# Optimization experiments

Measured on AMD Instinct MI355X. Metric: run time of the kernel, lower is better.

The kernel has to match this reference:

```python
import jax, jax.numpy as jnp
import numpy as np

B, V = 256, 128000


def setup_inputs() -> dict:
    key = jax.random.key(0)
    k1, k2, k3, k4, k5 = jax.random.split(key, 5)
    logits = jax.random.normal(k1, (B, V), dtype=jnp.float32) * 2.0
    temperatures = jax.random.uniform(k2, (B,), dtype=jnp.float32, minval=0.5, maxval=1.5)
    top_ps = jax.random.uniform(k3, (B,), dtype=jnp.float32, minval=0.7, maxval=1.0)
    top_ks = jax.random.randint(k4, (B,), 1, 101, dtype=jnp.int32)
    min_ps = jax.random.uniform(k5, (B,), dtype=jnp.float32, minval=0.0, maxval=0.1)
    return {"logits": logits, "temperatures": temperatures, "top_ps": top_ps,
            "top_ks": top_ks, "min_ps": min_ps}


def reference(logits, temperatures, top_ps, top_ks, min_ps):
    # temperature scaling + softmax (forward path with is_all_greedy=False)
    logits = logits.astype(jnp.float32) / temperatures[:, None]
    probs = jax.nn.softmax(logits, axis=-1)  # [B, V]

    # descending sort of probabilities, keep permutation for un-sorting
    order = jnp.argsort(-probs, axis=-1)                      # [B, V]
    probs_sort = jnp.take_along_axis(probs, order, axis=-1)   # [B, V]
    csum = jnp.cumsum(probs_sort, axis=-1)                    # cumsum BEFORE masking (matches torch)

    ranks = jnp.arange(V, dtype=jnp.int32)[None, :]
    probs_sort = jnp.where(ranks >= top_ks[:, None], 0.0, probs_sort)          # top-k mask
    probs_sort = jnp.where(csum - probs_sort > top_ps[:, None], 0.0, probs_sort)  # top-p mask
    # need_min_p_sampling=False in forward, so min_ps is unused (kept for signature parity)

    # multinomial(num_samples=1) over unnormalized masked probs == categorical on log-weights
    logw = jnp.where(probs_sort > 0, jnp.log(probs_sort), -jnp.inf)
    sampled = jax.random.categorical(jax.random.key(42), logw, axis=-1)  # [B]
    next_ids = jnp.take_along_axis(order, sampled[:, None], axis=-1).reshape(-1)
    return next_ids
```

## Files before the change

### kernel.cpp

```cpp
#include <hip/hip_runtime.h>
#include <stdint.h>
#include <math.h>

#define BB 256
#define VV 128000
#define NV4 (VV / 4)
#define NHALF4 (NV4 / 2)
#define CAPG 512
#define KMAX 100
#define TPB 1024
#define TPC 512
#define THR 6.0f
#define LOG2E 1.4426950408889634f

#define WS_CNT_OFF 0
#define WS_Z_OFF 1024
#define WS_CL_OFF 3072
#define WS_CI_OFF (3072 + BB * CAPG * 4)
#define WS_NEED (size_t)(3072 + BB * CAPG * 8)

__device__ __forceinline__ uint32_t threefry_xor_bits(uint32_t x0, uint32_t x1) {
    const uint32_t k0 = 0u, k1 = 42u;
    const uint32_t k2 = k0 ^ k1 ^ 0x1BD11BDAu;
    uint32_t ks[3] = {k0, k1, k2};
    const int rotA[4] = {13, 15, 26, 6};
    const int rotB[4] = {17, 29, 16, 24};
    x0 += ks[0];
    x1 += ks[1];
#pragma unroll
    for (int g = 0; g < 5; g++) {
        const int* rot = (g & 1) ? rotB : rotA;
#pragma unroll
        for (int i = 0; i < 4; i++) {
            x0 += x1;
            x1 = (x1 << rot[i]) | (x1 >> (32 - rot[i]));
            x1 ^= x0;
        }
        x0 += ks[(g + 1) % 3];
        x1 += ks[(g + 2) % 3] + (uint32_t)(g + 1);
    }
    return x0 ^ x1;
}

__device__ __forceinline__ float wave_maxf(float v) {
    for (int s = 32; s > 0; s >>= 1) v = fmaxf(v, __shfl_down(v, s));
    return v;
}
__device__ __forceinline__ float wave_sumf(float v) {
    for (int s = 32; s > 0; s >>= 1) v += __shfl_down(v, s);
    return v;
}

__device__ void common_tail(int b, int tid, const float* sort_p, const int* sort_idx,
                            float* csum_s, float* red_val, int* red_idx,
                            float topp, int topk, int* out) {
    if (tid == 0) {
        float c = 0.f;
        for (int r = 0; r < KMAX; r++) {
            c += sort_p[r];
            csum_s[r] = c;
        }
    }
    __syncthreads();
    float val = -INFINITY;
    if (tid < KMAX && tid < topk) {
        float p = sort_p[tid];
        if (!(csum_s[tid] - p > topp)) {
            float lw = logf(p);
            uint32_t idx = (uint32_t)b * (uint32_t)VV + (uint32_t)tid;
            uint32_t bits = threefry_xor_bits(0u, idx);
            uint32_t fb = (bits >> 9) | 0x3F800000u;
            float f = __uint_as_float(fb) - 1.0f;
            const float TINY = 1.17549435082228751e-38f;
            float u = fmaxf(TINY, __fadd_rn(__fmul_rn(f, 1.0f - TINY), TINY));
            float g = -logf(-logf(u));
            val = g + lw;
        }
    }
    if (tid < 128) {
        red_val[tid] = (tid < KMAX) ? val : -INFINITY;
        red_idx[tid] = tid;
    }
    __syncthreads();
    for (int s = 64; s > 0; s >>= 1) {
        if (tid < s) {
            float v1 = red_val[tid], v2 = red_val[tid + s];
            int i1 = red_idx[tid], i2 = red_idx[tid + s];
            if (v2 > v1 || (v2 == v1 && i2 < i1)) {
                red_val[tid] = v2;
                red_idx[tid] = i2;
            }
        }
        __syncthreads();
    }
    if (tid == 0) out[b] = sort_idx[red_idx[0]];
}

template <int NT>
__device__ void fallback_fill(const float* row, float T, int tid,
                              float* wv, int* iwv, float* sort_p, int* sort_idx,
                              float* s_f , int* s_i ) {
    const int lane = tid & 63, wave = tid >> 6;
    const int NW = NT / 64;
    float lm = -INFINITY;
    for (int j = tid; j < VV; j += NT) lm = fmaxf(lm, row[j]);
    lm = wave_maxf(lm);
    if (lane == 0) wv[wave] = lm;
    __syncthreads();
    if (tid == 0) {
        float M = wv[0];
        for (int w = 1; w < NW; w++) M = fmaxf(M, wv[w]);
        s_f[0] = M;
    }
    __syncthreads();
    const float m = s_f[0] / T;
    float zp = 0.f;
    for (int j = tid; j < VV; j += NT) zp += expf(row[j] / T - m);
    zp = wave_sumf(zp);
    __syncthreads();
    if (lane == 0) wv[wave] = zp;
    __syncthreads();
    if (tid == 0) {
        float Zs = wv[0];
        for (int w = 1; w < NW; w++) Zs += wv[w];
        s_f[1] = Zs;
    }
    __syncthreads();
    const float Z = s_f[1];
    float prevP = INFINITY;
    int prevJ = -1;
    for (int r = 0; r < KMAX; r++) {
        float bp = -1.f;
        int bj = 0x7FFFFFFF;
        for (int j = tid; j < VV; j += NT) {
            float p = expf(row[j] / T - m);
            bool elig = (p < prevP) || (p == prevP && j > prevJ);
            if (elig && (p > bp || (p == bp && j < bj))) {
                bp = p;
                bj = j;
            }
        }
        for (int s = 32; s > 0; s >>= 1) {
            float op = __shfl_down(bp, s);
            int oj = __shfl_down(bj, s);
            if (op > bp || (op == bp && oj < bj)) {
                bp = op;
                bj = oj;
            }
        }
        if (lane == 0) {
            wv[wave] = bp;
            iwv[wave] = bj;
        }
        __syncthreads();
        if (tid == 0) {
            float P = wv[0];
            int J = iwv[0];
            for (int w = 1; w < NW; w++)
                if (wv[w] > P || (wv[w] == P && iwv[w] < J)) {
                    P = wv[w];
                    J = iwv[w];
                }
            sort_p[r] = P / Z;
            sort_idx[r] = J;
            s_f[1] = P;
            s_i[0] = J;
        }
        __syncthreads();
        prevP = s_f[1];
        prevJ = s_i[0];
        __syncthreads();
    }
}

__global__ void init_kernel(int* wcnt) {
    if (threadIdx.x < BB) wcnt[threadIdx.x] = 0;
}

__global__ __launch_bounds__(TPB, 8) void pass_kernel(
    const float* __restrict__ logits, const float* __restrict__ temps,
    int* __restrict__ wcnt, float* __restrict__ wz,
    float* __restrict__ wcl, int* __restrict__ wci) {
    __shared__ float wv[TPB / 64];
    const int blk = blockIdx.x;
    const int b = blk >> 1, half = blk & 1;
    const int tid = threadIdx.x, lane = tid & 63, wave = tid >> 6;
    const float T = temps[b];
    const float c1 = LOG2E / T;
    const float4* row4 = (const float4*)(logits + (size_t)b * VV) + half * NHALF4;
    const int base4 = half * NHALF4;

    float z = 0.f;
    int i = tid;
    for (; i + 3 * TPB < NHALF4; i += 4 * TPB) {
        float4 v0 = row4[i];
        float4 v1 = row4[i + TPB];
        float4 v2 = row4[i + 2 * TPB];
        float4 v3 = row4[i + 3 * TPB];
        float a[16] = {v0.x, v0.y, v0.z, v0.w, v1.x, v1.y, v1.z, v1.w,
                       v2.x, v2.y, v2.z, v2.w, v3.x, v3.y, v3.z, v3.w};
#pragma unroll
        for (int j = 0; j < 16; j++) {
            float l = a[j];
            z += exp2f(l * c1);
            if (l >= THR) {
                int slot = atomicAdd(&wcnt[b], 1);
                if (slot < CAPG) {
                    wcl[b * CAPG + slot] = l;
                    wci[b * CAPG + slot] = (base4 + i + (j >> 2) * TPB) * 4 + (j & 3);
                }
            }
        }
    }
    for (; i < NHALF4; i += TPB) {
        float4 v = row4[i];
        float a[4] = {v.x, v.y, v.z, v.w};
#pragma unroll
        for (int j = 0; j < 4; j++) {
            float l = a[j];
            z += exp2f(l * c1);
            if (l >= THR) {
                int slot = atomicAdd(&wcnt[b], 1);
                if (slot < CAPG) {
                    wcl[b * CAPG + slot] = l;
                    wci[b * CAPG + slot] = (base4 + i) * 4 + j;
                }
            }
        }
    }
    z = wave_sumf(z);
    if (lane == 0) wv[wave] = z;
    __syncthreads();
    if (tid == 0) {
        float Z = wv[0];
        for (int w = 1; w < TPB / 64; w++) Z += wv[w];
        wz[2 * b + half] = Z;
    }
}

__global__ __launch_bounds__(TPC) void tail_kernel(
    const float* __restrict__ logits, const float* __restrict__ temps,
    const float* __restrict__ top_ps, const int* __restrict__ top_ks,
    const int* __restrict__ wcnt, const float* __restrict__ wz,
    const float* __restrict__ wcl, const int* __restrict__ wci,
    int* __restrict__ out) {
    __shared__ float cand_p[CAPG];
    __shared__ int cand_i[CAPG];
    __shared__ float sort_p[KMAX];
    __shared__ int sort_idx[KMAX];
    __shared__ float csum_s[KMAX];
    __shared__ float red_val[128];
    __shared__ int red_idx[128];
    __shared__ float wv[TPC / 64];
    __shared__ int iwv[TPC / 64];
    __shared__ float s_f[2];
    __shared__ int s_i[1];

    const int b = blockIdx.x, tid = threadIdx.x, lane = tid & 63, wave = tid >> 6;
    const float T = temps[b];
    const float c1 = LOG2E / T;
    const int cnt = wcnt[b];
    const float* row = logits + (size_t)b * VV;

    if (cnt >= KMAX && cnt <= CAPG) {
        const int C = cnt;
        float myl = -INFINITY;
        int myi = 0;
        if (tid < C) {
            myl = wcl[b * CAPG + tid];
            myi = wci[b * CAPG + tid];
        }
        float v = wave_maxf(myl);
        if (lane == 0) wv[wave] = v;
        __syncthreads();
        if (tid == 0) {
            float M = wv[0];
            for (int w = 1; w < TPC / 64; w++) M = fmaxf(M, wv[w]);
            s_f[0] = M;
        }
        __syncthreads();
        const float lmax = s_f[0];
        const float m = lmax / T;
        const float Z = (wz[2 * b] + wz[2 * b + 1]) * exp2f(-lmax * c1);
        float my_pn = 0.f;
        if (tid < C) {
            float x = myl / T;
            float p = expf(x - m);
            my_pn = p / Z;
            cand_p[tid] = my_pn;
            cand_i[tid] = myi;
        }
        __syncthreads();
        if (tid < C) {
            int r = 0;
            for (int c = 0; c < C; c++) {
                float pc = cand_p[c];
                int ic = cand_i[c];
                if (pc > my_pn || (pc == my_pn && ic < myi)) r++;
            }
            if (r < KMAX) {
                sort_p[r] = my_pn;
                sort_idx[r] = myi;
            }
        }
        __syncthreads();
    } else {
        fallback_fill<TPC>(row, T, tid, wv, iwv, sort_p, sort_idx, s_f, s_i);
    }

    common_tail(b, tid, sort_p, sort_idx, csum_s, red_val, red_idx,
                top_ps[b], top_ks[b], out);
}

__global__ __launch_bounds__(TPB) void fused_kernel(
    const float* __restrict__ logits, const float* __restrict__ temps,
    const float* __restrict__ top_ps, const int* __restrict__ top_ks,
    int* __restrict__ out) {
    __shared__ float cl[CAPG];
    __shared__ int ci[CAPG];
    __shared__ float cand_p[CAPG];
    __shared__ int cand_i[CAPG];
    __shared__ float sort_p[KMAX];
    __shared__ int sort_idx[KMAX];
    __shared__ float csum_s[KMAX];
    __shared__ float red_val[128];
    __shared__ int red_idx[128];
    __shared__ float wv[TPB / 64];
    __shared__ int iwv[TPB / 64];
    __shared__ float s_f[2];
    __shared__ int s_i[1];
    __shared__ int s_cnt;

    const int b = blockIdx.x, tid = threadIdx.x, lane = tid & 63, wave = tid >> 6;
    const float T = temps[b];
    const float c1 = LOG2E / T;
    const float* row = logits + (size_t)b * VV;
    const float4* row4 = (const float4*)row;

    if (tid == 0) s_cnt = 0;
    __syncthreads();
    float z = 0.f, lmax = -INFINITY;
    for (int i = tid; i < NV4; i += TPB) {
        float4 v = row4[i];
        float a[4] = {v.x, v.y, v.z, v.w};
#pragma unroll
        for (int j = 0; j < 4; j++) {
            float l = a[j];
            lmax = fmaxf(lmax, l);
            z += exp2f(l * c1);
            if (l >= THR) {
                int slot = atomicAdd(&s_cnt, 1);
                if (slot < CAPG) {
                    cl[slot] = l;
                    ci[slot] = i * 4 + j;
                }
            }
        }
    }
    lmax = wave_maxf(lmax);
    if (lane == 0) wv[wave] = lmax;
    __syncthreads();
    if (tid == 0) {
        float M = wv[0];
        for (int w = 1; w < TPB / 64; w++) M = fmaxf(M, wv[w]);
        s_f[0] = M;
    }
    __syncthreads();
    const float lm = s_f[0];
    z = wave_sumf(z);
    __syncthreads();
    if (lane == 0) wv[wave] = z;
    __syncthreads();
    if (tid == 0) {
        float Zs = wv[0];
        for (int w = 1; w < TPB / 64; w++) Zs += wv[w];
        s_f[1] = Zs;
    }
    __syncthreads();
    const float Zraw = s_f[1];
    const int cnt = s_cnt;
    __syncthreads();

    if (cnt >= KMAX && cnt <= CAPG) {
        const int C = cnt;
        const float m = lm / T;
        const float Z = Zraw * exp2f(-lm * c1);
        float my_pn = 0.f;
        int myi = 0;
        if (tid < C) {
            float x = cl[tid] / T;
            float p = expf(x - m);
            my_pn = p / Z;
            myi = ci[tid];
            cand_p[tid] = my_pn;
            cand_i[tid] = myi;
        }
        __syncthreads();
        if (tid < C) {
            int r = 0;
            for (int c = 0; c < C; c++) {
                float pc = cand_p[c];
                int icx = cand_i[c];
                if (pc > my_pn || (pc == my_pn && icx < myi)) r++;
            }
            if (r < KMAX) {
                sort_p[r] = my_pn;
                sort_idx[r] = myi;
            }
        }
        __syncthreads();
    } else {
        fallback_fill<TPB>(row, T, tid, wv, iwv, sort_p, sort_idx, s_f, s_i);
    }

    common_tail(b, tid, sort_p, sort_idx, csum_s, red_val, red_idx,
                top_ps[b], top_ks[b], out);
}

extern "C" void kernel_launch(void* const* d_in, const int* in_sizes, int n_in,
                              void* d_out, int out_size, void* d_ws, size_t ws_size,
                              hipStream_t stream) {
    const float* logits = (const float*)d_in[0];
    const float* temps = (const float*)d_in[1];
    const float* top_ps = (const float*)d_in[2];
    const int* top_ks = (const int*)d_in[3];
    int* out = (int*)d_out;

    if (ws_size >= WS_NEED) {
        char* wsb = (char*)d_ws;
        int* wcnt = (int*)(wsb + WS_CNT_OFF);
        float* wz = (float*)(wsb + WS_Z_OFF);
        float* wcl = (float*)(wsb + WS_CL_OFF);
        int* wci = (int*)(wsb + WS_CI_OFF);
        init_kernel<<<1, 256, 0, stream>>>(wcnt);
        pass_kernel<<<BB * 2, TPB, 0, stream>>>(logits, temps, wcnt, wz, wcl, wci);
        tail_kernel<<<BB, TPC, 0, stream>>>(logits, temps, top_ps, top_ks,
                                            wcnt, wz, wcl, wci, out);
    } else {
        fused_kernel<<<BB, TPB, 0, stream>>>(logits, temps, top_ps, top_ks, out);
    }
}
```

Before: 238.8 us.

## Split rows into eight slices with shared-memory candidate buffers, drop init kernel

The pass kernel now splits each row into eight slices handled by 256-thread blocks instead of two halves on 1024-thread blocks. Candidates above the threshold are gathered into per-block shared memory with shared atomics, then written out with per-slice counts. This removes global atomics and the separate init kernel. A max-of-16 early check skips the per-element candidate test for most groups. The tail kernel merges the eight slice lists and sums eight partial Z values, which adds a little serial work per row.

```diff
diff --git a/kernel.cpp b/kernel.cpp
--- a/kernel.cpp
+++ b/kernel.cpp
@@ -5,19 +5,23 @@
 #define BB 256
 #define VV 128000
 #define NV4 (VV / 4)
-#define NHALF4 (NV4 / 2)
+#define SLICES 8
+#define SLICE_E (VV / SLICES)
+#define SLICE_F4 (SLICE_E / 4)
+#define SL 320
 #define CAPG 512
 #define KMAX 100
+#define TPP 256
+#define TPC 512
 #define TPB 1024
-#define TPC 512
 #define THR 6.0f
 #define LOG2E 1.4426950408889634f
 
 #define WS_CNT_OFF 0
-#define WS_Z_OFF 1024
-#define WS_CL_OFF 3072
-#define WS_CI_OFF (3072 + BB * CAPG * 4)
-#define WS_NEED (size_t)(3072 + BB * CAPG * 8)
+#define WS_Z_OFF 8192
+#define WS_CL_OFF 16384
+#define WS_CI_OFF (16384 + 2048 * SL * 4)
+#define WS_NEED (size_t)(16384 + (size_t)2048 * SL * 8)
 
 __device__ __forceinline__ uint32_t threefry_xor_bits(uint32_t x0, uint32_t x1) {
     const uint32_t k0 = 0u, k1 = 42u;
@@ -99,7 +103,7 @@
 template <int NT>
 __device__ void fallback_fill(const float* row, float T, int tid,
                               float* wv, int* iwv, float* sort_p, int* sort_idx,
-                              float* s_f , int* s_i ) {
+                              float* s_f, int* s_i) {
     const int lane = tid & 63, wave = tid >> 6;
     const int NW = NT / 64;
     float lm = -INFINITY;
@@ -173,68 +177,89 @@
     }
 }
 
-__global__ void init_kernel(int* wcnt) {
-    if (threadIdx.x < BB) wcnt[threadIdx.x] = 0;
-}
-
-__global__ __launch_bounds__(TPB, 8) void pass_kernel(
+__global__ __launch_bounds__(TPP, 8) void pass_kernel(
     const float* __restrict__ logits, const float* __restrict__ temps,
     int* __restrict__ wcnt, float* __restrict__ wz,
     float* __restrict__ wcl, int* __restrict__ wci) {
-    __shared__ float wv[TPB / 64];
+    __shared__ float scl[SL];
+    __shared__ int sci[SL];
+    __shared__ float wvv[TPP / 64];
+    __shared__ int s_cnt;
+
     const int blk = blockIdx.x;
-    const int b = blk >> 1, half = blk & 1;
+    const int b = blk >> 3, sl = blk & 7;
     const int tid = threadIdx.x, lane = tid & 63, wave = tid >> 6;
     const float T = temps[b];
     const float c1 = LOG2E / T;
-    const float4* row4 = (const float4*)(logits + (size_t)b * VV) + half * NHALF4;
-    const int base4 = half * NHALF4;
+    const float4* row4 = (const float4*)(logits + (size_t)b * VV) + sl * SLICE_F4;
+    const int ebase = sl * SLICE_E;
+
+    if (tid == 0) s_cnt = 0;
+    __syncthreads();
 
     float z = 0.f;
     int i = tid;
-    for (; i + 3 * TPB < NHALF4; i += 4 * TPB) {
+    for (; i + 3 * TPP < SLICE_F4; i += 4 * TPP) {
         float4 v0 = row4[i];
-        float4 v1 = row4[i + TPB];
-        float4 v2 = row4[i + 2 * TPB];
-        float4 v3 = row4[i + 3 * TPB];
-        float a[16] = {v0.x, v0.y, v0.z, v0.w, v1.x, v1.y, v1.z, v1.w,
-                       v2.x, v2.y, v2.z, v2.w, v3.x, v3.y, v3.z, v3.w};
+        float4 v1 = row4[i + TPP];
+        float4 v2 = row4[i + 2 * TPP];
+        float4 v3 = row4[i + 3 * TPP];
+        float b0 = fmaxf(fmaxf(v0.x, v0.y), fmaxf(v0.z, v0.w));
+        float b1 = fmaxf(fmaxf(v1.x, v1.y), fmaxf(v1.z, v1.w));
+        float b2 = fmaxf(fmaxf(v2.x, v2.y), fmaxf(v2.z, v2.w));
+        float b3 = fmaxf(fmaxf(v3.x, v3.y), fmaxf(v3.z, v3.w));
+        float bmax = fmaxf(fmaxf(b0, b1), fmaxf(b2, b3));
+        float e0 = (exp2f(v0.x * c1) + exp2f(v0.y * c1)) + (exp2f(v0.z * c1) + exp2f(v0.w * c1));
+        float e1 = (exp2f(v1.x * c1) + exp2f(v1.y * c1)) + (exp2f(v1.z * c1) + exp2f(v1.w * c1));
+        float e2 = (exp2f(v2.x * c1) + exp2f(v2.y * c1)) + (exp2f(v2.z * c1) + exp2f(v2.w * c1));
+        float e3 = (exp2f(v3.x * c1) + exp2f(v3.y * c1)) + (exp2f(v3.z * c1) + exp2f(v3.w * c1));
+        z += (e0 + e1) + (e2 + e3);
+        if (bmax >= THR) {
+            float a[16] = {v0.x, v0.y, v0.z, v0.w, v1.x, v1.y, v1.z, v1.w,
+                           v2.x, v2.y, v2.z, v2.w, v3.x, v3.y, v3.z, v3.w};
 #pragma unroll
-        for (int j = 0; j < 16; j++) {
-            float l = a[j];
-            z += exp2f(l * c1);
-            if (l >= THR) {
-                int slot = atomicAdd(&wcnt[b], 1);
-                if (slot < CAPG) {
-                    wcl[b * CAPG + slot] = l;
-                    wci[b * CAPG + slot] = (base4 + i + (j >> 2) * TPB) * 4 + (j & 3);
+            for (int j = 0; j < 16; j++) {
+                if (a[j] >= THR) {
+                    int slot = atomicAdd(&s_cnt, 1);
+                    if (slot < SL) {
+                        scl[slot] = a[j];
+                        sci[slot] = ebase + (i + (j >> 2) * TPP) * 4 + (j & 3);
+                    }
                 }
             }
         }
     }
-    for (; i < NHALF4; i += TPB) {
+    for (; i < SLICE_F4; i += TPP) {
         float4 v = row4[i];
-        float a[4] = {v.x, v.y, v.z, v.w};
+        float bmax = fmaxf(fmaxf(v.x, v.y), fmaxf(v.z, v.w));
+        z += (exp2f(v.x * c1) + exp2f(v.y * c1)) + (exp2f(v.z * c1) + exp2f(v.w * c1));
+        if (bmax >= THR) {
+            float a[4] = {v.x, v.y, v.z, v.w};
 #pragma unroll
-        for (int j = 0; j < 4; j++) {
-            float l = a[j];
-            z += exp2f(l * c1);
-            if (l >= THR) {
-                int slot = atomicAdd(&wcnt[b], 1);
-                if (slot < CAPG) {
-                    wcl[b * CAPG + slot] = l;
-                    wci[b * CAPG + slot] = (base4 + i) * 4 + j;
+            for (int j = 0; j < 4; j++) {
+                if (a[j] >= THR) {
+                    int slot = atomicAdd(&s_cnt, 1);
+                    if (slot < SL) {
+                        scl[slot] = a[j];
+                        sci[slot] = ebase + i * 4 + j;
+                    }
                 }
             }
         }
     }
     z = wave_sumf(z);
-    if (lane == 0) wv[wave] = z;
-    __syncthreads();
-    if (tid == 0) {
-        float Z = wv[0];
-        for (int w = 1; w < TPB / 64; w++) Z += wv[w];
-        wz[2 * b + half] = Z;
+    if (lane == 0) wvv[wave] = z;
+    __syncthreads();
+    if (tid == 0) {
+        float Zs = wvv[0];
+        for (int w = 1; w < TPP / 64; w++) Zs += wvv[w];
+        wz[blk] = Zs;
+        wcnt[blk] = s_cnt;
+    }
+    const int n = (s_cnt < SL) ? s_cnt : SL;
+    for (int k = tid; k < n; k += TPP) {
+        wcl[blk * SL + k] = scl[k];
+        wci[blk * SL + k] = sci[k];
     }
 }
 
@@ -244,6 +269,7 @@
     const int* __restrict__ wcnt, const float* __restrict__ wz,
     const float* __restrict__ wcl, const int* __restrict__ wci,
     int* __restrict__ out) {
+    __shared__ float cand_l[CAPG];
     __shared__ float cand_p[CAPG];
     __shared__ int cand_i[CAPG];
     __shared__ float sort_p[KMAX];
@@ -255,20 +281,46 @@
     __shared__ int iwv[TPC / 64];
     __shared__ float s_f[2];
     __shared__ int s_i[1];
+    __shared__ int soff[SLICES];
+    __shared__ int scnts[SLICES];
+    __shared__ int s_stat;
 
     const int b = blockIdx.x, tid = threadIdx.x, lane = tid & 63, wave = tid >> 6;
     const float T = temps[b];
     const float c1 = LOG2E / T;
-    const int cnt = wcnt[b];
     const float* row = logits + (size_t)b * VV;
 
-    if (cnt >= KMAX && cnt <= CAPG) {
-        const int C = cnt;
+    if (tid == 0) {
+        int o = 0, bad = 0;
+        for (int s = 0; s < SLICES; s++) {
+            int c = wcnt[b * SLICES + s];
+            scnts[s] = c;
+            soff[s] = o;
+            o += c;
+            if (c > SL) bad = 1;
+        }
+        if (o < KMAX || o > CAPG) bad = 1;
+        s_i[0] = o;
+        s_stat = bad;
+    }
+    __syncthreads();
+    const int C = s_i[0];
+    const int bad = s_stat;
+
+    if (!bad) {
+        for (int s = 0; s < SLICES; s++) {
+            const int base = (b * SLICES + s) * SL, o = soff[s], c = scnts[s];
+            for (int k = tid; k < c; k += TPC) {
+                cand_l[o + k] = wcl[base + k];
+                cand_i[o + k] = wci[base + k];
+            }
+        }
+        __syncthreads();
         float myl = -INFINITY;
         int myi = 0;
         if (tid < C) {
-            myl = wcl[b * CAPG + tid];
-            myi = wci[b * CAPG + tid];
+            myl = cand_l[tid];
+            myi = cand_i[tid];
         }
         float v = wave_maxf(myl);
         if (lane == 0) wv[wave] = v;
@@ -281,14 +333,20 @@
         __syncthreads();
         const float lmax = s_f[0];
         const float m = lmax / T;
-        const float Z = (wz[2 * b] + wz[2 * b + 1]) * exp2f(-lmax * c1);
+        float Zraw;
+        if (tid == 0) {
+            Zraw = 0.f;
+            for (int s = 0; s < SLICES; s++) Zraw += wz[b * SLICES + s];
+            s_f[1] = Zraw;
+        }
+        __syncthreads();
+        const float Z = s_f[1] * exp2f(-lmax * c1);
         float my_pn = 0.f;
         if (tid < C) {
             float x = myl / T;
             float p = expf(x - m);
             my_pn = p / Z;
             cand_p[tid] = my_pn;
-            cand_i[tid] = myi;
         }
         __syncthreads();
         if (tid < C) {
@@ -432,8 +490,7 @@
         float* wz = (float*)(wsb + WS_Z_OFF);
         float* wcl = (float*)(wsb + WS_CL_OFF);
         int* wci = (int*)(wsb + WS_CI_OFF);
-        init_kernel<<<1, 256, 0, stream>>>(wcnt);
-        pass_kernel<<<BB * 2, TPB, 0, stream>>>(logits, temps, wcnt, wz, wcl, wci);
+        pass_kernel<<<BB * SLICES, TPP, 0, stream>>>(logits, temps, wcnt, wz, wcl, wci);
         tail_kernel<<<BB, TPC, 0, stream>>>(logits, temps, top_ps, top_ks,
                                             wcnt, wz, wcl, wci, out);
     } else {
```

Result: faster. 223.2 us (-6.5%).
